# Kernel tuning notes

Measured on AMD Instinct MI355X. Metric: run time of the kernel, lower is better.

## Reference

```python
import jax, jax.numpy as jnp
import numpy as np

N_FFT = 256
HOP = 128
TOP_K = 2


def _stft_mag(x):
    # torch.stft(center=True, pad_mode='reflect') with periodic hann window
    pad = N_FFT // 2
    xp = jnp.pad(x, ((0, 0), (pad, pad)), mode='reflect')
    n_frames = 1 + (xp.shape[1] - N_FFT) // HOP
    idx = jnp.arange(n_frames)[:, None] * HOP + jnp.arange(N_FFT)[None, :]
    frames = xp[:, idx]                              # [B, T, n_fft]
    win = 0.5 * (1.0 - jnp.cos(2.0 * jnp.pi * jnp.arange(N_FFT) / N_FFT))
    spec = jnp.fft.rfft(frames * win, axis=-1)       # [B, T, F]
    return jnp.abs(spec).transpose(0, 2, 1)          # [B, F, T]


def setup_inputs() -> dict:
    key = jax.random.key(0)
    ks = jax.random.split(key, 4)
    B, L, E, D, H, F = 256, 4096, 8, 1024, 128, N_FFT // 2 + 1
    x = jax.random.normal(ks[0], (B, L), dtype=jnp.float32)
    gate_w1 = jax.random.normal(ks[1], (F, H), dtype=jnp.float32) * (1.0 / np.sqrt(F))
    gate_b1 = jnp.zeros((H,), dtype=jnp.float32)
    gate_w2 = jax.random.normal(ks[2], (H, E), dtype=jnp.float32) * (1.0 / np.sqrt(H))
    gate_b2 = jnp.zeros((E,), dtype=jnp.float32)
    expert_w = jax.random.normal(ks[3], (E, L, D), dtype=jnp.float32) * (1.0 / np.sqrt(L))
    expert_b = jnp.zeros((E, D), dtype=jnp.float32)
    return {"x": x, "gate_w1": gate_w1, "gate_b1": gate_b1,
            "gate_w2": gate_w2, "gate_b2": gate_b2,
            "expert_w": expert_w, "expert_b": expert_b}


def reference(x, gate_w1, gate_b1, gate_w2, gate_b2, expert_w, expert_b):
    B = x.shape[0]
    # --- frequency-domain gating (STFT is under no_grad in the original) ---
    mag = jax.lax.stop_gradient(_stft_mag(x))        # [B, F, T]
    pooled = mag.mean(axis=-1)                       # adaptive_avg_pool1d(.,1)  [B, F]
    h = jax.nn.relu(pooled @ gate_w1 + gate_b1)
    logits = h @ gate_w2 + gate_b2                   # [B, E]
    top_vals, top_idx = jax.lax.top_k(logits, TOP_K) # [B, k]
    weights = jax.nn.softmax(top_vals, axis=1)       # [B, k]
    # --- time-domain experts (dense per-expert GEMM) ---
    expert_out = jnp.einsum('bl,eld->ebd', x, expert_w) + expert_b[:, None, :]  # [E, B, D]
    # --- fused gather + weighted combine (replaces the python double loop) ---
    gathered = expert_out[top_idx, jnp.arange(B)[:, None]]  # [B, k, D]
    return jnp.einsum('bk,bkd->bd', weights, gathered)      # [B, D]
```

## Files before the change

kernel.cpp:

```cpp
#include <hip/hip_runtime.h>
#include <hip/hip_bf16.h>

typedef __bf16 bf16v8 __attribute__((ext_vector_type(8)));
typedef float f32v4 __attribute__((ext_vector_type(4)));

#define PI2F 6.28318530717958647692f

__device__ __forceinline__ int skew_i(int k) { return k + (k >> 5); }

__global__ __launch_bounds__(128) void k_stft(const float* __restrict__ x,
    float* __restrict__ pp, __hip_bfloat16* __restrict__ xb,
    float* __restrict__ eo)
{
  const int bx = blockIdx.x;
  const int b = bx >> 2, q = bx & 3;
  const int tid = threadIdx.x;
  __shared__ __align__(16) float xrow[4096];
  __shared__ float ctab[264];
  __shared__ __align__(16) float vwp[132];
  __shared__ __align__(16) float vwm[132];
  __shared__ float red[2];

  {
    f32v4 z = {0.f, 0.f, 0.f, 0.f};
    f32v4* p = (f32v4*)eo + (size_t)bx * 512;
#pragma unroll
    for (int i = 0; i < 4; ++i) p[tid + i * 128] = z;
  }
  for (int k = tid; k < 256; k += 128)
    ctab[skew_i(k)] = cosf(PI2F * (1.0f / 256.0f) * (float)k);
  {
    const float4* xv = (const float4*)(x + (size_t)b * 4096);
    float4* xl = (float4*)xrow;
#pragma unroll
    for (int i = 0; i < 8; ++i) xl[tid + i * 128] = xv[tid + i * 128];
  }
  __syncthreads();
  {
    int c0 = q * 1024 + tid * 8;
    __align__(16) __hip_bfloat16 tmp[8];
#pragma unroll
    for (int j = 0; j < 8; ++j) tmp[j] = __float2bfloat16(xrow[c0 + j]);
    *(bf16v8*)(xb + (size_t)b * 4096 + c0) = *(bf16v8*)tmp;
  }

  const int f = tid + 1;
  const float cf = ctab[skew_i(f)];
  const float sf = ctab[skew_i((f + 192) & 255)];
  const int k16 = (16 * f) & 255;
  float accf = 0.f, acc0 = 0.f;
  const int t0 = q * 8;
  const int t1 = (q == 3) ? 33 : (t0 + 8);

  for (int t = t0; t < t1; ++t) {
    float v0, v1;
    {
      int p_ = t * 128 + tid;
      int xi = (p_ < 128) ? (128 - p_) : ((p_ < 4224) ? (p_ - 128) : (8318 - p_));
      v0 = xrow[xi] * (0.5f - 0.5f * ctab[skew_i(tid)]);
      p_ += 128;
      xi = (p_ < 128) ? (128 - p_) : ((p_ < 4224) ? (p_ - 128) : (8318 - p_));
      v1 = xrow[xi] * (0.5f - 0.5f * ctab[skew_i(tid + 128)]);
    }
    __syncthreads();
    vwp[tid] = v0 + v1;
    vwm[tid] = v0 - v1;
    float s = v0 + v1;
#pragma unroll
    for (int o = 32; o; o >>= 1) s += __shfl_down(s, o);
    if ((tid & 63) == 0) red[tid >> 6] = s;
    __syncthreads();
    if (tid == 0) acc0 += fabsf(red[0] + red[1]);

    const float* vsrc = (f & 1) ? vwm : vwp;
    float re = 0.f, im = 0.f;
    int k0 = 0;
#pragma unroll 1
    for (int j = 0; j < 8; ++j) {
      float wr = ctab[skew_i(k0)];
      float wi = -ctab[skew_i((k0 + 192) & 255)];
      const float4* vp = (const float4*)(vsrc + j * 16);
#pragma unroll
      for (int u = 0; u < 4; ++u) {
        float4 v4 = vp[u];
        float t2;
        re += v4.x * wr; im += v4.x * wi; t2 = wr*cf + wi*sf; wi = wi*cf - wr*sf; wr = t2;
        re += v4.y * wr; im += v4.y * wi; t2 = wr*cf + wi*sf; wi = wi*cf - wr*sf; wr = t2;
        re += v4.z * wr; im += v4.z * wi; t2 = wr*cf + wi*sf; wi = wi*cf - wr*sf; wr = t2;
        re += v4.w * wr; im += v4.w * wi; t2 = wr*cf + wi*sf; wi = wi*cf - wr*sf; wr = t2;
      }
      k0 = (k0 + k16) & 255;
    }
    accf += sqrtf(re * re + im * im);
  }
  pp[(size_t)(q * 256 + b) * 132 + f] = accf;
  if (tid == 0) pp[(size_t)(q * 256 + b) * 132] = acc0;
}

__global__ __launch_bounds__(128) void k_gate(const float* __restrict__ pp,
    const float* __restrict__ w1, const float* __restrict__ b1,
    const float* __restrict__ w2, const float* __restrict__ b2,
    int2* __restrict__ gidx, float2* __restrict__ gw)
{
  const int b = blockIdx.x, tid = threadIdx.x;
  __shared__ float pl[129];
  __shared__ float hh[128];
  __shared__ float lgt[8];
  for (int ff = tid; ff < 129; ff += 128) {
    float s = 0.f;
#pragma unroll
    for (int qq = 0; qq < 4; ++qq) s += pp[(size_t)(qq * 256 + b) * 132 + ff];
    pl[ff] = s * (1.0f / 33.0f);
  }
  __syncthreads();
  float h = b1[tid];
  for (int ff = 0; ff < 129; ++ff) h += pl[ff] * w1[ff * 128 + tid];
  hh[tid] = fmaxf(h, 0.f);
  __syncthreads();
  if (tid < 8) {
    float l = b2[tid];
    for (int j = 0; j < 128; ++j) l += hh[j] * w2[j * 8 + tid];
    lgt[tid] = l;
  }
  __syncthreads();
  if (tid == 0) {
    int i0 = 0; float v0 = lgt[0];
#pragma unroll
    for (int i = 1; i < 8; ++i) if (lgt[i] > v0) { v0 = lgt[i]; i0 = i; }
    int i1 = -1; float v1 = -3.4e38f;
#pragma unroll
    for (int i = 0; i < 8; ++i) { if (i == i0) continue; if (lgt[i] > v1) { v1 = lgt[i]; i1 = i; } }
    float e1 = expf(v1 - v0);
    float wA = 1.0f / (1.0f + e1);
    gidx[b] = make_int2(i0, i1);
    gw[b] = make_float2(wA, e1 * wA);
  }
}

__global__ __launch_bounds__(256) void k_gemm(const __hip_bfloat16* __restrict__ xb,
    const float* __restrict__ W, float* __restrict__ eo)
{
  const int bx = blockIdx.x;
  const int ks = bx & 3, nt = (bx >> 2) & 15, e = bx >> 6;
  const int n0 = nt * 64;
  const int kbase = ks * 1024;
  const int tid = threadIdx.x;
  const int w = tid >> 6, l = tid & 63;
  const int lr = l & 15, lgp = l >> 4;
  __shared__ __hip_bfloat16 XL[256][40];
  __shared__ __hip_bfloat16 WL[64][40];
  f32v4 acc[4][4];
  f32v4 z = {0.f, 0.f, 0.f, 0.f};
#pragma unroll
  for (int m = 0; m < 4; ++m)
#pragma unroll
    for (int nb = 0; nb < 4; ++nb) acc[m][nb] = z;
  const float* Wp = W + ((size_t)e << 22) + n0;
  const int sx_seg = tid & 3, sx_row = tid >> 2;
  const int sw_n = tid & 63, sw_k4 = tid >> 6;
  for (int kc = 0; kc < 32; ++kc) {
    const int kb = kbase + kc * 32;
#pragma unroll
    for (int p = 0; p < 4; ++p) {
      int row = p * 64 + sx_row;
      *(bf16v8*)(&XL[row][sx_seg * 8]) =
          *(const bf16v8*)(xb + (size_t)row * 4096 + kb + sx_seg * 8);
    }
#pragma unroll
    for (int p = 0; p < 8; ++p) {
      int kk = p * 4 + sw_k4;
      WL[sw_n][kk] = __float2bfloat16(Wp[(size_t)(kb + kk) * 1024 + sw_n]);
    }
    __syncthreads();
    bf16v8 af[4], bfr[4];
#pragma unroll
    for (int m = 0; m < 4; ++m)
      af[m] = *(const bf16v8*)(&XL[w * 64 + m * 16 + lr][lgp * 8]);
#pragma unroll
    for (int nb = 0; nb < 4; ++nb)
      bfr[nb] = *(const bf16v8*)(&WL[nb * 16 + lr][lgp * 8]);
#pragma unroll
    for (int m = 0; m < 4; ++m)
#pragma unroll
      for (int nb = 0; nb < 4; ++nb)
        acc[m][nb] = __builtin_amdgcn_mfma_f32_16x16x32_bf16(af[m], bfr[nb], acc[m][nb], 0, 0, 0);
    __syncthreads();
  }
#pragma unroll
  for (int m = 0; m < 4; ++m)
#pragma unroll
    for (int nb = 0; nb < 4; ++nb)
#pragma unroll
      for (int r = 0; r < 4; ++r) {
        int row = w * 64 + m * 16 + lgp * 4 + r;
        int col = n0 + nb * 16 + lr;
        atomicAdd(eo + ((size_t)e * 256 + row) * 1024 + col, acc[m][nb][r]);
      }
}

__global__ __launch_bounds__(256) void k_gather(const float* __restrict__ eo,
    const float* __restrict__ eb, const int2* __restrict__ gidx,
    const float2* __restrict__ gw, float* __restrict__ out)
{
  const int b = blockIdx.x, tid = threadIdx.x;
  const int2 ii = gidx[b];
  const float2 wwv = gw[b];
  const float4* r0 = (const float4*)(eo + ((size_t)ii.x * 256 + b) * 1024);
  const float4* r1 = (const float4*)(eo + ((size_t)ii.y * 256 + b) * 1024);
  const float4* b0 = (const float4*)(eb + (size_t)ii.x * 1024);
  const float4* b1p = (const float4*)(eb + (size_t)ii.y * 1024);
  float4* op = (float4*)(out + (size_t)b * 1024);
  float4 a = r0[tid], c = r1[tid], ba = b0[tid], bc = b1p[tid];
  float4 o;
  o.x = wwv.x * (a.x + ba.x) + wwv.y * (c.x + bc.x);
  o.y = wwv.x * (a.y + ba.y) + wwv.y * (c.y + bc.y);
  o.z = wwv.x * (a.z + ba.z) + wwv.y * (c.z + bc.z);
  o.w = wwv.x * (a.w + ba.w) + wwv.y * (c.w + bc.w);
  op[tid] = o;
}

extern "C" void kernel_launch(void* const* d_in, const int* in_sizes, int n_in,
                              void* d_out, int out_size, void* d_ws, size_t ws_size,
                              hipStream_t stream) {
  const float* x  = (const float*)d_in[0];
  const float* w1 = (const float*)d_in[1];
  const float* b1 = (const float*)d_in[2];
  const float* w2 = (const float*)d_in[3];
  const float* b2 = (const float*)d_in[4];
  const float* W  = (const float*)d_in[5];
  const float* eb = (const float*)d_in[6];
  float* out = (float*)d_out;
  char* ws = (char*)d_ws;

  float* eo            = (float*)ws;
  __hip_bfloat16* xb   = (__hip_bfloat16*)(ws + 8388608);
  float* pp            = (float*)(ws + 8388608 + 2097152);
  int2* gidx           = (int2*)(ws + 8388608 + 2097152 + 540672);
  float2* gw           = (float2*)(ws + 8388608 + 2097152 + 540672 + 2048);

  hipLaunchKernelGGL(k_stft,   dim3(1024), dim3(128), 0, stream, x, pp, xb, eo);
  hipLaunchKernelGGL(k_gate,   dim3(256),  dim3(128), 0, stream, pp, w1, b1, w2, b2, gidx, gw);
  hipLaunchKernelGGL(k_gemm,   dim3(512),  dim3(256), 0, stream, xb, W, eo);
  hipLaunchKernelGGL(k_gather, dim3(256),  dim3(256), 0, stream, eo, eb, gidx, gw, out);
}
```

Baseline: 304.5 us.

## Route tokens sparsely per expert and fuse weighted combine into GEMM epilogue

The gate kernel now builds per-expert lists of routed token indices and weights with atomic counters, and writes the bias-weighted combine directly into the output. The GEMM gathers only routed rows through global_load_lds and skips empty M-tiles. Its epilogue atomically adds the weighted results straight into the output, which removes the dense [E,B,D] intermediate, its zeroing and the separate gather kernel. W is read with float4 loads into a pre-swizzled MFMA layout on a finer N tiling, and the STFT processes four frames per synchronisation with independent accumulators. The cost is atomic-dependent routing and non-deterministic float accumulation order.

Result: faster. 273.1 us (-10.3%).

```diff
diff --git a/kernel.cpp b/kernel.cpp
--- a/kernel.cpp
+++ b/kernel.cpp
@@ -3,30 +3,31 @@
 
 typedef __bf16 bf16v8 __attribute__((ext_vector_type(8)));
 typedef float f32v4 __attribute__((ext_vector_type(4)));
+typedef unsigned int u32;
 
 #define PI2F 6.28318530717958647692f
-
 __device__ __forceinline__ int skew_i(int k) { return k + (k >> 5); }
+
+#define GLL16(g, s) __builtin_amdgcn_global_load_lds( \
+    (const __attribute__((address_space(1))) u32*)(g), \
+    (__attribute__((address_space(3))) u32*)(s), 16, 0, 0)
 
 __global__ __launch_bounds__(128) void k_stft(const float* __restrict__ x,
     float* __restrict__ pp, __hip_bfloat16* __restrict__ xb,
-    float* __restrict__ eo)
+    int* __restrict__ ridx ,
+    int* __restrict__ cnt)
 {
-  const int bx = blockIdx.x;
-  const int b = bx >> 2, q = bx & 3;
-  const int tid = threadIdx.x;
+  const int bx = blockIdx.x, b = bx >> 2, q = bx & 3, tid = threadIdx.x;
   __shared__ __align__(16) float xrow[4096];
   __shared__ float ctab[264];
-  __shared__ __align__(16) float vwp[132];
-  __shared__ __align__(16) float vwm[132];
-  __shared__ float red[2];
-
-  {
-    f32v4 z = {0.f, 0.f, 0.f, 0.f};
-    f32v4* p = (f32v4*)eo + (size_t)bx * 512;
-#pragma unroll
-    for (int i = 0; i < 4; ++i) p[tid + i * 128] = z;
-  }
+  __shared__ __align__(16) float vwp4[128][4];
+  __shared__ __align__(16) float vwm4[128][4];
+  __shared__ __align__(16) float red[2][4];
+
+  if (bx < 16)
+    ((float2*)((char*)ridx + (size_t)bx * 1024))[tid] = make_float2(0.f, 0.f);
+  if (bx == 16 && tid < 8) cnt[tid] = 0;
+
   for (int k = tid; k < 256; k += 128)
     ctab[skew_i(k)] = cosf(PI2F * (1.0f / 256.0f) * (float)k);
   {
@@ -49,49 +50,59 @@
   const float sf = ctab[skew_i((f + 192) & 255)];
   const int k16 = (16 * f) & 255;
   float accf = 0.f, acc0 = 0.f;
-  const int t0 = q * 8;
-  const int t1 = (q == 3) ? 33 : (t0 + 8);
-
-  for (int t = t0; t < t1; ++t) {
-    float v0, v1;
-    {
-      int p_ = t * 128 + tid;
-      int xi = (p_ < 128) ? (128 - p_) : ((p_ < 4224) ? (p_ - 128) : (8318 - p_));
-      v0 = xrow[xi] * (0.5f - 0.5f * ctab[skew_i(tid)]);
-      p_ += 128;
-      xi = (p_ < 128) ? (128 - p_) : ((p_ < 4224) ? (p_ - 128) : (8318 - p_));
-      v1 = xrow[xi] * (0.5f - 0.5f * ctab[skew_i(tid + 128)]);
-    }
-    __syncthreads();
-    vwp[tid] = v0 + v1;
-    vwm[tid] = v0 - v1;
-    float s = v0 + v1;
-#pragma unroll
-    for (int o = 32; o; o >>= 1) s += __shfl_down(s, o);
-    if ((tid & 63) == 0) red[tid >> 6] = s;
-    __syncthreads();
-    if (tid == 0) acc0 += fabsf(red[0] + red[1]);
-
-    const float* vsrc = (f & 1) ? vwm : vwp;
-    float re = 0.f, im = 0.f;
+  const int nGroups = (q == 3) ? 3 : 2;
+
+  for (int g = 0; g < nGroups; ++g) {
+    float vp_[4], vm_[4], sm_[4];
+#pragma unroll
+    for (int fr = 0; fr < 4; ++fr) {
+      int t = q * 8 + g * 4 + fr;
+      float v0 = 0.f, v1 = 0.f;
+      if (t < 33) {
+        int p_ = t * 128 + tid;
+        int xi = (p_ < 128) ? (128 - p_) : ((p_ < 4224) ? (p_ - 128) : (8318 - p_));
+        v0 = xrow[xi] * (0.5f - 0.5f * ctab[skew_i(tid)]);
+        p_ += 128;
+        xi = (p_ < 128) ? (128 - p_) : ((p_ < 4224) ? (p_ - 128) : (8318 - p_));
+        v1 = xrow[xi] * (0.5f - 0.5f * ctab[skew_i(tid + 128)]);
+      }
+      vp_[fr] = v0 + v1; vm_[fr] = v0 - v1; sm_[fr] = v0 + v1;
+    }
+#pragma unroll
+    for (int o = 32; o; o >>= 1) {
+#pragma unroll
+      for (int fr = 0; fr < 4; ++fr) sm_[fr] += __shfl_down(sm_[fr], o);
+    }
+    __syncthreads();
+    *(float4*)&vwp4[tid][0] = make_float4(vp_[0], vp_[1], vp_[2], vp_[3]);
+    *(float4*)&vwm4[tid][0] = make_float4(vm_[0], vm_[1], vm_[2], vm_[3]);
+    if ((tid & 63) == 0)
+      *(float4*)&red[tid >> 6][0] = make_float4(sm_[0], sm_[1], sm_[2], sm_[3]);
+    __syncthreads();
+    if (tid == 0) {
+#pragma unroll
+      for (int fr = 0; fr < 4; ++fr) acc0 += fabsf(red[0][fr] + red[1][fr]);
+    }
+    const float4* vsrc = (const float4*)((f & 1) ? &vwm4[0][0] : &vwp4[0][0]);
+    float re0 = 0, im0 = 0, re1 = 0, im1 = 0, re2 = 0, im2 = 0, re3 = 0, im3 = 0;
     int k0 = 0;
 #pragma unroll 1
     for (int j = 0; j < 8; ++j) {
       float wr = ctab[skew_i(k0)];
       float wi = -ctab[skew_i((k0 + 192) & 255)];
-      const float4* vp = (const float4*)(vsrc + j * 16);
-#pragma unroll
-      for (int u = 0; u < 4; ++u) {
-        float4 v4 = vp[u];
-        float t2;
-        re += v4.x * wr; im += v4.x * wi; t2 = wr*cf + wi*sf; wi = wi*cf - wr*sf; wr = t2;
-        re += v4.y * wr; im += v4.y * wi; t2 = wr*cf + wi*sf; wi = wi*cf - wr*sf; wr = t2;
-        re += v4.z * wr; im += v4.z * wi; t2 = wr*cf + wi*sf; wi = wi*cf - wr*sf; wr = t2;
-        re += v4.w * wr; im += v4.w * wi; t2 = wr*cf + wi*sf; wi = wi*cf - wr*sf; wr = t2;
+#pragma unroll
+      for (int u = 0; u < 16; ++u) {
+        float4 a = vsrc[j * 16 + u];
+        re0 += a.x * wr; im0 += a.x * wi;
+        re1 += a.y * wr; im1 += a.y * wi;
+        re2 += a.z * wr; im2 += a.z * wi;
+        re3 += a.w * wr; im3 += a.w * wi;
+        float t2 = wr * cf + wi * sf; wi = wi * cf - wr * sf; wr = t2;
       }
       k0 = (k0 + k16) & 255;
     }
-    accf += sqrtf(re * re + im * im);
+    accf += sqrtf(re0 * re0 + im0 * im0) + sqrtf(re1 * re1 + im1 * im1)
+          + sqrtf(re2 * re2 + im2 * im2) + sqrtf(re3 * re3 + im3 * im3);
   }
   pp[(size_t)(q * 256 + b) * 132 + f] = accf;
   if (tid == 0) pp[(size_t)(q * 256 + b) * 132] = acc0;
@@ -100,12 +111,16 @@
 __global__ __launch_bounds__(128) void k_gate(const float* __restrict__ pp,
     const float* __restrict__ w1, const float* __restrict__ b1,
     const float* __restrict__ w2, const float* __restrict__ b2,
-    int2* __restrict__ gidx, float2* __restrict__ gw)
+    const float* __restrict__ eb,
+    int* __restrict__ ridx, float* __restrict__ rw, int* __restrict__ cnt,
+    float* __restrict__ out)
 {
   const int b = blockIdx.x, tid = threadIdx.x;
   __shared__ float pl[129];
   __shared__ float hh[128];
   __shared__ float lgt[8];
+  __shared__ int sIdx[2];
+  __shared__ float sW[2];
   for (int ff = tid; ff < 129; ff += 128) {
     float s = 0.f;
 #pragma unroll
@@ -132,91 +147,121 @@
     for (int i = 0; i < 8; ++i) { if (i == i0) continue; if (lgt[i] > v1) { v1 = lgt[i]; i1 = i; } }
     float e1 = expf(v1 - v0);
     float wA = 1.0f / (1.0f + e1);
-    gidx[b] = make_int2(i0, i1);
-    gw[b] = make_float2(wA, e1 * wA);
-  }
-}
-
-__global__ __launch_bounds__(256) void k_gemm(const __hip_bfloat16* __restrict__ xb,
-    const float* __restrict__ W, float* __restrict__ eo)
+    float wB = e1 * wA;
+    sIdx[0] = i0; sIdx[1] = i1; sW[0] = wA; sW[1] = wB;
+    int s0 = atomicAdd(&cnt[i0], 1); ridx[i0 * 256 + s0] = b; rw[i0 * 256 + s0] = wA;
+    int s1 = atomicAdd(&cnt[i1], 1); ridx[i1 * 256 + s1] = b; rw[i1 * 256 + s1] = wB;
+  }
+  __syncthreads();
+  const float4* e0 = (const float4*)(eb + (size_t)sIdx[0] * 1024);
+  const float4* e1p = (const float4*)(eb + (size_t)sIdx[1] * 1024);
+  const float wA = sW[0], wB = sW[1];
+  float4* op = (float4*)(out + (size_t)b * 1024);
+#pragma unroll
+  for (int i = 0; i < 2; ++i) {
+    float4 a = e0[tid + i * 128], c = e1p[tid + i * 128];
+    float4 o;
+    o.x = wA * a.x + wB * c.x; o.y = wA * a.y + wB * c.y;
+    o.z = wA * a.z + wB * c.z; o.w = wA * a.w + wB * c.w;
+    op[tid + i * 128] = o;
+  }
+}
+
+__global__ __launch_bounds__(256, 4) void k_gemm(const __hip_bfloat16* __restrict__ xb,
+    const float* __restrict__ W, const int* __restrict__ ridx,
+    const float* __restrict__ rw, const int* __restrict__ cnt,
+    float* __restrict__ out)
 {
   const int bx = blockIdx.x;
-  const int ks = bx & 3, nt = (bx >> 2) & 15, e = bx >> 6;
-  const int n0 = nt * 64;
-  const int kbase = ks * 1024;
-  const int tid = threadIdx.x;
-  const int w = tid >> 6, l = tid & 63;
+  const int ks = bx & 3, nt = (bx >> 2) & 31, e = bx >> 7;
+  const int cntE = cnt[e];
+  if (cntE == 0) return;
+  const int tid = threadIdx.x, w = tid >> 6, l = tid & 63;
   const int lr = l & 15, lgp = l >> 4;
-  __shared__ __hip_bfloat16 XL[256][40];
-  __shared__ __hip_bfloat16 WL[64][40];
-  f32v4 acc[4][4];
-  f32v4 z = {0.f, 0.f, 0.f, 0.f};
-#pragma unroll
-  for (int m = 0; m < 4; ++m)
-#pragma unroll
-    for (int nb = 0; nb < 4; ++nb) acc[m][nb] = z;
-  const float* Wp = W + ((size_t)e << 22) + n0;
-  const int sx_seg = tid & 3, sx_row = tid >> 2;
-  const int sw_n = tid & 63, sw_k4 = tid >> 6;
-  for (int kc = 0; kc < 32; ++kc) {
-    const int kb = kbase + kc * 32;
-#pragma unroll
-    for (int p = 0; p < 4; ++p) {
-      int row = p * 64 + sx_row;
-      *(bf16v8*)(&XL[row][sx_seg * 8]) =
-          *(const bf16v8*)(xb + (size_t)row * 4096 + kb + sx_seg * 8);
-    }
-#pragma unroll
-    for (int p = 0; p < 8; ++p) {
-      int kk = p * 4 + sw_k4;
-      WL[sw_n][kk] = __float2bfloat16(Wp[(size_t)(kb + kk) * 1024 + sw_n]);
-    }
-    __syncthreads();
-    bf16v8 af[4], bfr[4];
-#pragma unroll
-    for (int m = 0; m < 4; ++m)
-      af[m] = *(const bf16v8*)(&XL[w * 64 + m * 16 + lr][lgp * 8]);
-#pragma unroll
-    for (int nb = 0; nb < 4; ++nb)
-      bfr[nb] = *(const bf16v8*)(&WL[nb * 16 + lr][lgp * 8]);
-#pragma unroll
-    for (int m = 0; m < 4; ++m)
-#pragma unroll
-      for (int nb = 0; nb < 4; ++nb)
-        acc[m][nb] = __builtin_amdgcn_mfma_f32_16x16x32_bf16(af[m], bfr[nb], acc[m][nb], 0, 0, 0);
-    __syncthreads();
-  }
-#pragma unroll
-  for (int m = 0; m < 4; ++m)
-#pragma unroll
-    for (int nb = 0; nb < 4; ++nb)
-#pragma unroll
-      for (int r = 0; r < 4; ++r) {
-        int row = w * 64 + m * 16 + lgp * 4 + r;
-        int col = n0 + nb * 16 + lr;
-        atomicAdd(eo + ((size_t)e * 256 + row) * 1024 + col, acc[m][nb][r]);
-      }
-}
-
-__global__ __launch_bounds__(256) void k_gather(const float* __restrict__ eo,
-    const float* __restrict__ eb, const int2* __restrict__ gidx,
-    const float2* __restrict__ gw, float* __restrict__ out)
-{
-  const int b = blockIdx.x, tid = threadIdx.x;
-  const int2 ii = gidx[b];
-  const float2 wwv = gw[b];
-  const float4* r0 = (const float4*)(eo + ((size_t)ii.x * 256 + b) * 1024);
-  const float4* r1 = (const float4*)(eo + ((size_t)ii.y * 256 + b) * 1024);
-  const float4* b0 = (const float4*)(eb + (size_t)ii.x * 1024);
-  const float4* b1p = (const float4*)(eb + (size_t)ii.y * 1024);
-  float4* op = (float4*)(out + (size_t)b * 1024);
-  float4 a = r0[tid], c = r1[tid], ba = b0[tid], bc = b1p[tid];
-  float4 o;
-  o.x = wwv.x * (a.x + ba.x) + wwv.y * (c.x + bc.x);
-  o.y = wwv.x * (a.y + ba.y) + wwv.y * (c.y + bc.y);
-  o.z = wwv.x * (a.z + ba.z) + wwv.y * (c.z + bc.z);
-  o.w = wwv.x * (a.w + ba.w) + wwv.y * (c.w + bc.w);
-  op[tid] = o;
+  __shared__ __align__(16) __hip_bfloat16 XLf[16384];
+  __shared__ __align__(16) __hip_bfloat16 WLf[2048];
+
+  u32 xoff[8];
+#pragma unroll
+  for (int i = 0; i < 8; ++i) {
+    int mts = (w * 8 + i) >> 1;
+    int ksd = i & 1;
+    int row = mts * 16 + lr;
+    int bRow = ridx[e * 256 + row];
+    xoff[i] = (u32)bRow * 8192u + (u32)ks * 2048u + (u32)ksd * 64u + (u32)lgp * 16u;
+  }
+  const char* xbB = (const char*)xb;
+  char* XLb = (char*)XLf;
+  const int k2 = tid >> 3, nseg = tid & 7;
+  const float* Wp = W + ((size_t)e << 22) + ((size_t)ks << 20) + nt * 32 + nseg * 4;
+
+  f32v4 acc[4][2];
+  const f32v4 z = {0.f, 0.f, 0.f, 0.f};
+#pragma unroll
+  for (int m = 0; m < 4; ++m) { acc[m][0] = z; acc[m][1] = z; }
+
+  for (int kc = 0; kc < 16; ++kc) {
+    float4 Wa = *(const float4*)(Wp + (size_t)(kc * 64 + 2 * k2) * 1024);
+    float4 Wb = *(const float4*)(Wp + (size_t)(kc * 64 + 2 * k2) * 1024 + 1024);
+    const u32 kcb = (u32)kc * 128u;
+#pragma unroll
+    for (int i = 0; i < 8; ++i) {
+      int mts = (w * 8 + i) >> 1;
+      if (mts * 16 < cntE)
+        GLL16(xbB + xoff[i] + kcb, XLb + ((w * 8 + i) << 10));
+    }
+    {
+      int kk = 2 * k2;
+      int ksd = kk >> 5, lgpd = (kk >> 3) & 3, wsl = k2 & 3;
+      float a_[4] = {Wa.x, Wa.y, Wa.z, Wa.w};
+      float b_[4] = {Wb.x, Wb.y, Wb.z, Wb.w};
+#pragma unroll
+      for (int i = 0; i < 4; ++i) {
+        int n = nseg * 4 + i;
+        int ntile = n >> 4, lrd = n & 15;
+        union { __hip_bfloat16 h[2]; u32 u; } pk;
+        pk.h[0] = __float2bfloat16(a_[i]);
+        pk.h[1] = __float2bfloat16(b_[i]);
+        ((u32*)WLf)[((((ntile * 2 + ksd) << 6) + (lgpd << 4) + lrd) << 2) + wsl] = pk.u;
+      }
+    }
+    __syncthreads();
+    bf16v8 bfr[2][2];
+#pragma unroll
+    for (int nb = 0; nb < 2; ++nb)
+#pragma unroll
+      for (int ksd = 0; ksd < 2; ++ksd)
+        bfr[nb][ksd] = *(const bf16v8*)((const char*)WLf + (((((nb * 2 + ksd) << 6) + l)) << 4));
+#pragma unroll
+    for (int m = 0; m < 4; ++m) {
+      int mt = m * 4 + w;
+      if (mt * 16 < cntE) {
+#pragma unroll
+        for (int ksd = 0; ksd < 2; ++ksd) {
+          bf16v8 af = *(const bf16v8*)(XLb + (((((mt * 2 + ksd) << 6) + l)) << 4));
+          acc[m][0] = __builtin_amdgcn_mfma_f32_16x16x32_bf16(af, bfr[0][ksd], acc[m][0], 0, 0, 0);
+          acc[m][1] = __builtin_amdgcn_mfma_f32_16x16x32_bf16(af, bfr[1][ksd], acc[m][1], 0, 0, 0);
+        }
+      }
+    }
+    __syncthreads();
+  }
+#pragma unroll
+  for (int m = 0; m < 4; ++m) {
+    int mt = m * 4 + w;
+    if (mt * 16 >= cntE) continue;
+#pragma unroll
+    for (int r = 0; r < 4; ++r) {
+      int row = mt * 16 + lgp * 4 + r;
+      float wgt = rw[e * 256 + row];
+      if (wgt != 0.f) {
+        int bRow = ridx[e * 256 + row];
+        float* o = out + (size_t)bRow * 1024 + nt * 32 + lr;
+        atomicAdd(o, acc[m][0][r] * wgt);
+        atomicAdd(o + 16, acc[m][1][r] * wgt);
+      }
+    }
+  }
 }
 
 extern "C" void kernel_launch(void* const* d_in, const int* in_sizes, int n_in,
@@ -232,14 +277,13 @@
   float* out = (float*)d_out;
   char* ws = (char*)d_ws;
 
-  float* eo            = (float*)ws;
-  __hip_bfloat16* xb   = (__hip_bfloat16*)(ws + 8388608);
-  float* pp            = (float*)(ws + 8388608 + 2097152);
-  int2* gidx           = (int2*)(ws + 8388608 + 2097152 + 540672);
-  float2* gw           = (float2*)(ws + 8388608 + 2097152 + 540672 + 2048);
-
-  hipLaunchKernelGGL(k_stft,   dim3(1024), dim3(128), 0, stream, x, pp, xb, eo);
-  hipLaunchKernelGGL(k_gate,   dim3(256),  dim3(128), 0, stream, pp, w1, b1, w2, b2, gidx, gw);
-  hipLaunchKernelGGL(k_gemm,   dim3(512),  dim3(256), 0, stream, xb, W, eo);
-  hipLaunchKernelGGL(k_gather, dim3(256),  dim3(256), 0, stream, eo, eb, gidx, gw, out);
-}
+  __hip_bfloat16* xb = (__hip_bfloat16*)ws;
+  float* pp  = (float*)(ws + 2097152);
+  int*   ridx = (int*)(ws + 2097152 + 540672);
+  float* rw   = (float*)(ws + 2097152 + 540672 + 8192);
+  int*   cnt  = (int*)(ws + 2097152 + 540672 + 16384);
+
+  hipLaunchKernelGGL(k_stft, dim3(1024), dim3(128), 0, stream, x, pp, xb, ridx, cnt);
+  hipLaunchKernelGGL(k_gate, dim3(256), dim3(128), 0, stream, pp, w1, b1, w2, b2, eb, ridx, rw, cnt, out);
+  hipLaunchKernelGGL(k_gemm, dim3(1024), dim3(256), 0, stream, xb, W, ridx, rw, cnt, out);
+}
```
